# Optimization experiments

Hardware: AMD Instinct MI355X
Metric: run time of the kernel (lower is better)

## Reference

```python
import jax, jax.numpy as jnp
import numpy as np

B, C, H, W = 8, 512, 48, 48
DK = C // 8            # query/key dim
L = max(H, W)          # rel_pos_length == H == W
R = 2 * L - 1          # num relative shifts
N = H * W
EPS = 1e-5


def setup_inputs() -> dict:
    key = jax.random.key(0)
    ks = jax.random.split(key, 20)
    d = {
        "x": jax.random.normal(ks[0], (B, C, H, W), jnp.float32),
        "Wq": jax.random.normal(ks[1], (DK, C), jnp.float32) * 0.02,
        "bq": jnp.zeros((DK,), jnp.float32),
        "q_scale": jnp.ones((DK,), jnp.float32),
        "q_bias": jnp.zeros((DK,), jnp.float32),
        "Wk": jax.random.normal(ks[2], (DK, C), jnp.float32) * 0.02,
        "bk": jnp.zeros((DK,), jnp.float32),
        "k_scale": jnp.ones((DK,), jnp.float32),
        "k_bias": jnp.zeros((DK,), jnp.float32),
        "Wv": jax.random.normal(ks[3], (C, C), jnp.float32) * 0.02,
        "bv": jnp.zeros((C,), jnp.float32),
        "v_scale": jnp.ones((C,), jnp.float32),
        "v_bias": jnp.zeros((C,), jnp.float32),
        "rel_rows": jax.random.normal(ks[4], (R, DK), jnp.float32),
        "rel_columns": jax.random.normal(ks[5], (R, DK), jnp.float32),
        "bnr_scale": jnp.ones((C,), jnp.float32),
        "bnr_bias": jnp.zeros((C,), jnp.float32),
        "bnc_scale": jnp.ones((C,), jnp.float32),
        "bnc_bias": jnp.zeros((C,), jnp.float32),
        # gamma is a learned scalar (init 0 in torch; nonzero here so output != x)
        "gamma": jax.random.normal(ks[6], (1,), jnp.float32) * 0.1,
    }
    return d


def _bn(y, scale, bias):
    # train-mode BatchNorm2d: batch stats over (B,H,W), biased variance
    m = jnp.mean(y, axis=(0, 2, 3))
    v = jnp.mean((y - m[None, :, None, None]) ** 2, axis=(0, 2, 3))
    yn = (y - m[None, :, None, None]) * jax.lax.rsqrt(v + EPS)[None, :, None, None]
    return yn * scale[None, :, None, None] + bias[None, :, None, None]


def _conv_bn_relu(x, Wc, bc, scale, bias):
    y = jnp.einsum('bchw,oc->bohw', x, Wc) + bc[None, :, None, None]  # 1x1 conv
    return jax.nn.relu(_bn(y, scale, bias))


def _rel_P(l, rel_table):
    # compute_reindexing_tensor reduces to a one-hot over shift (i - x) since
    # |i-x| <= L always holds when L == l; Ih @ rel_table == gather by shift.
    x = jnp.arange(l)[:, None]
    i = jnp.arange(l)[None, :]
    idx = i - x + (L - 1)                 # (l, l) in [0, 2L-2]
    return rel_table[idx]                 # (l, l, DK)


def reference(x, Wq, bq, q_scale, q_bias, Wk, bk, k_scale, k_bias,
              Wv, bv, v_scale, v_bias, rel_rows, rel_columns,
              bnr_scale, bnr_bias, bnc_scale, bnc_bias, gamma):
    q = _conv_bn_relu(x, Wq, bq, q_scale, q_bias).reshape(B, DK, N)   # proj_query^T
    k = _conv_bn_relu(x, Wk, bk, k_scale, k_bias).reshape(B, DK, N)
    v = _conv_bn_relu(x, Wv, bv, v_scale, v_bias).reshape(B, C, N)

    energy = jnp.einsum('bdn,bdm->bnm', q, k)        # (B,N,N) = Q^T K (unscaled)
    attention = jax.nn.softmax(energy, axis=-1)
    out = jnp.einsum('bcj,bij->bci', v, attention)   # V A^T
    attn_mask = out.reshape(B, C, H, W)

    # relative position terms: Eh = V (Ph Q^T), Ew = V (Pw Q^T)
    Ph = _rel_P(H, rel_rows).reshape(N, DK)          # (N,DK) since H==W
    Mh = jnp.einsum('nd,bdm->bnm', Ph, q)
    Eh = jnp.einsum('bcn,bnm->bcm', v, Mh).reshape(B, C, H, W)
    Eh = _bn(Eh, bnr_scale, bnr_bias)

    Pw = _rel_P(W, rel_columns).reshape(N, DK)
    Mw = jnp.einsum('nd,bdm->bnm', Pw, q)
    Ew = jnp.einsum('bcn,bnm->bcm', v, Mw).reshape(B, C, H, W)
    Ew = _bn(Ew, bnc_scale, bnc_bias)

    attn_mask = attn_mask + Eh + Ew
    return gamma[0] * attn_mask + x
```

## Files before the change

kernel.cpp:

```cpp
#include <hip/hip_runtime.h>
#include <math.h>

#define BB   8
#define CIN  512
#define NSP  2304
#define OCH  640
#define LL   48

typedef __attribute__((ext_vector_type(8))) short bf16x8;
typedef __attribute__((ext_vector_type(4))) float f32x4;

__device__ inline unsigned short f2bf(float f) {
  unsigned int u = __float_as_uint(f);
  unsigned int r = (u + 0x7fffu + ((u >> 16) & 1u)) >> 16;
  return (unsigned short)r;
}
__device__ inline float bf2f(unsigned short h) {
  return __uint_as_float(((unsigned int)h) << 16);
}

#define STAGE128x64(GP, LD, LDSN)                                              \
  {                                                                            \
    const unsigned short* gsrc_ = (GP);                                        \
    _Pragma("unroll") for (int cc_ = 0; cc_ < 4; cc_++) {                      \
      int base_ = w * 2048 + cc_ * 512;                                        \
      int row_ = w * 32 + cc_ * 8 + rsub;                                      \
      __builtin_amdgcn_global_load_lds(                                        \
          (const __attribute__((address_space(1))) void*)(gsrc_ +              \
              (size_t)row_ * (LD) + colb),                                     \
          (__attribute__((address_space(3))) void*)&LDSN[base_], 16, 0, 0);    \
    }                                                                          \
  }

#define MFMA128x128x64()                                                       \
  _Pragma("unroll") for (int kk_ = 0; kk_ < 2; kk_++) {                        \
    bf16x8 af_[4], bf_[4];                                                     \
    int kcol_ = kk_ * 32 + (lane >> 4) * 8;                                    \
    _Pragma("unroll") for (int m_ = 0; m_ < 4; m_++)                           \
      af_[m_] = *(const bf16x8*)&As[(wr * 64 + m_ * 16 + (lane & 15)) * 64 + kcol_]; \
    _Pragma("unroll") for (int n_ = 0; n_ < 4; n_++)                           \
      bf_[n_] = *(const bf16x8*)&Bs[(wc * 64 + n_ * 16 + (lane & 15)) * 64 + kcol_]; \
    _Pragma("unroll") for (int m_ = 0; m_ < 4; m_++)                           \
      _Pragma("unroll") for (int n_ = 0; n_ < 4; n_++)                         \
        acc[m_][n_] = __builtin_amdgcn_mfma_f32_16x16x32_bf16(                 \
            af_[m_], bf_[n_], acc[m_][n_], 0, 0, 0);                           \
  }

#define MFMA_PROLOG()                                                          \
  const int tid = threadIdx.x;                                                 \
  const int lane = tid & 63;                                                   \
  const int w = tid >> 6;                                                      \
  const int wr = w >> 1, wc = w & 1;                                           \
  const int colb = (lane & 7) * 8;                                             \
  const int rsub = lane >> 3;                                                  \
  f32x4 acc[4][4] = {};                                                        \
  (void)colb; (void)rsub;

__global__ __launch_bounds__(256) void stack_wb(
    const float* __restrict__ Wq, const float* __restrict__ bq,
    const float* __restrict__ Wk, const float* __restrict__ bk,
    const float* __restrict__ Wv, const float* __restrict__ bv,
    unsigned short* __restrict__ Wstb, float* __restrict__ bst) {
  int idx = blockIdx.x * 256 + threadIdx.x;
  int row = idx >> 9;
  float val;
  if (row < 64)       val = Wq[idx];
  else if (row < 128) val = Wk[idx - (64 << 9)];
  else                val = Wv[idx - (128 << 9)];
  Wstb[idx] = f2bf(val);
  if (idx < OCH) {
    float bval;
    if (idx < 64)       bval = bq[idx];
    else if (idx < 128) bval = bk[idx - 64];
    else                bval = bv[idx - 128];
    bst[idx] = bval;
  }
}

__global__ __launch_bounds__(256) void prep_pcat(
    const float* __restrict__ rel_rows, const float* __restrict__ rel_cols,
    unsigned short* __restrict__ Pcatb) {
  int idx = blockIdx.x * 256 + threadIdx.x;
  int dd = idx / NSP;
  int n = idx - dd * NSP;
  int xr = n / LL;
  int ic = n - xr * LL;
  int shift = ic - xr + (LL - 1);
  float val = (dd < 64) ? rel_rows[shift * 64 + dd] : rel_cols[shift * 64 + (dd - 64)];
  Pcatb[idx] = f2bf(val);
}

__global__ __launch_bounds__(256) void transpose_x(
    const float* __restrict__ x, unsigned short* __restrict__ xTb) {
  __shared__ float t[64][65];
  const int n0 = blockIdx.x * 64;
  const int c0 = blockIdx.y * 64;
  const int b = blockIdx.z;
  const int j = threadIdx.x & 63;
  const int g = threadIdx.x >> 6;
  const float* xp = x + (size_t)b * CIN * NSP;
#pragma unroll
  for (int i = 0; i < 16; i++) {
    int cl = g * 16 + i;
    t[cl][j] = xp[(size_t)(c0 + cl) * NSP + n0 + j];
  }
  __syncthreads();
  unsigned short* op = xTb + (size_t)b * NSP * CIN;
#pragma unroll
  for (int i = 0; i < 16; i++) {
    int nl = g * 16 + i;
    op[(size_t)(n0 + nl) * CIN + c0 + j] = f2bf(t[j][nl]);
  }
}

__global__ __launch_bounds__(256) void proj_mfma(
    const unsigned short* __restrict__ Wstb, const float* __restrict__ bst,
    const unsigned short* __restrict__ xTb, unsigned short* __restrict__ y16,
    float* __restrict__ part1, float* __restrict__ part2) {
  __shared__ unsigned short As[128 * 64];
  __shared__ unsigned short Bs[128 * 64];
  int sw = ((blockIdx.x & 7) * 90) + (blockIdx.x >> 3);
  const int rb = sw % 5;
  const int nb = (sw / 5) % 18;
  const int b = sw / 90;
  const int r0 = rb * 128;
  const int n0 = nb * 128;
  MFMA_PROLOG();
  const unsigned short* A = Wstb + (size_t)r0 * CIN;
  const unsigned short* B = xTb + (size_t)b * NSP * CIN + (size_t)n0 * CIN;
  for (int k0 = 0; k0 < CIN; k0 += 64) {
    STAGE128x64(A + k0, CIN, As);
    STAGE128x64(B + k0, CIN, Bs);
    __syncthreads();
    MFMA128x128x64();
    __syncthreads();
  }
  float* sp = (float*)As;
#pragma unroll
  for (int m = 0; m < 4; m++) {
#pragma unroll
    for (int r = 0; r < 4; r++) {
      int rl = wr * 64 + m * 16 + (lane >> 4) * 4 + r;
      int row = r0 + rl;
      float bias = bst[row];
      float s1 = 0.f, s2 = 0.f;
#pragma unroll
      for (int n = 0; n < 4; n++) {
        float yv = acc[m][n][r] + bias;
        s1 += yv;
        s2 += yv * yv;
        y16[((size_t)b * OCH + row) * NSP + n0 + wc * 64 + n * 16 + (lane & 15)] = f2bf(yv);
      }
#pragma unroll
      for (int off = 1; off < 16; off <<= 1) {
        s1 += __shfl_xor(s1, off);
        s2 += __shfl_xor(s2, off);
      }
      if ((lane & 15) == 0) {
        sp[rl * 2 + wc] = s1;
        sp[256 + rl * 2 + wc] = s2;
      }
    }
  }
  __syncthreads();
  if (tid < 128) {
    size_t pbase = ((size_t)b * 18 + nb) * OCH + r0 + tid;
    part1[pbase] = sp[tid * 2] + sp[tid * 2 + 1];
    part2[pbase] = sp[256 + tid * 2] + sp[256 + tid * 2 + 1];
  }
}

__global__ __launch_bounds__(256) void bn_finalize(
    const float* __restrict__ part1, const float* __restrict__ part2,
    const float* __restrict__ qs_, const float* __restrict__ qb_,
    const float* __restrict__ ks_, const float* __restrict__ kb_,
    const float* __restrict__ vs_, const float* __restrict__ vb_,
    float* __restrict__ chanA, float* __restrict__ chanB) {
  const int ch = blockIdx.x;
  const int tid = threadIdx.x;
  float s1 = 0.f, s2 = 0.f;
  for (int t = tid; t < 144; t += 256) {
    s1 += part1[(size_t)t * OCH + ch];
    s2 += part2[(size_t)t * OCH + ch];
  }
  __shared__ float sb[8];
#pragma unroll
  for (int off = 32; off > 0; off >>= 1) {
    s1 += __shfl_down(s1, off);
    s2 += __shfl_down(s2, off);
  }
  int lane = tid & 63, wid = tid >> 6;
  if (lane == 0) { sb[wid] = s1; sb[4 + wid] = s2; }
  __syncthreads();
  if (tid == 0) {
    float ts  = sb[0] + sb[1] + sb[2] + sb[3];
    float ts2 = sb[4] + sb[5] + sb[6] + sb[7];
    const float inv = 1.f / (float)(BB * NSP);
    float mean = ts * inv;
    float var  = ts2 * inv - mean * mean;
    float scale, bias;
    if (ch < 64)       { scale = qs_[ch];       bias = qb_[ch]; }
    else if (ch < 128) { scale = ks_[ch - 64];  bias = kb_[ch - 64]; }
    else               { scale = vs_[ch - 128]; bias = vb_[ch - 128]; }
    float a = scale * rsqrtf(var + 1e-5f);
    chanA[ch] = a;
    chanB[ch] = bias - mean * a;
  }
}

__global__ __launch_bounds__(256) void bnrelu_all(
    unsigned short* __restrict__ y16, const float* __restrict__ chanA,
    const float* __restrict__ chanB) {
  size_t i = ((size_t)blockIdx.x * 256 + threadIdx.x) * 8;
  int ch = (int)((i / NSP) % OCH);
  float a = chanA[ch], bo = chanB[ch];
  ushort4 u0 = *(ushort4*)&y16[i];
  ushort4 u1 = *(ushort4*)&y16[i + 4];
  ushort4 o0, o1;
  o0.x = f2bf(fmaxf(0.f, a * bf2f(u0.x) + bo));
  o0.y = f2bf(fmaxf(0.f, a * bf2f(u0.y) + bo));
  o0.z = f2bf(fmaxf(0.f, a * bf2f(u0.z) + bo));
  o0.w = f2bf(fmaxf(0.f, a * bf2f(u0.w) + bo));
  o1.x = f2bf(fmaxf(0.f, a * bf2f(u1.x) + bo));
  o1.y = f2bf(fmaxf(0.f, a * bf2f(u1.y) + bo));
  o1.z = f2bf(fmaxf(0.f, a * bf2f(u1.z) + bo));
  o1.w = f2bf(fmaxf(0.f, a * bf2f(u1.w) + bo));
  *(ushort4*)&y16[i] = o0;
  *(ushort4*)&y16[i + 4] = o1;
}

__global__ __launch_bounds__(256) void tr_qk(
    const unsigned short* __restrict__ y16, unsigned short* __restrict__ qTb,
    unsigned short* __restrict__ kTb) {
  __shared__ unsigned short t[64][72];
  const int n0 = blockIdx.x * 64;
  const int qk = blockIdx.y;
  const int b = blockIdx.z;
  const int j = threadIdx.x & 63;
  const int g = threadIdx.x >> 6;
#pragma unroll
  for (int i = 0; i < 16; i++) {
    int cl = g * 16 + i;
    t[cl][j] = y16[((size_t)b * OCH + qk * 64 + cl) * NSP + n0 + j];
  }
  __syncthreads();
  unsigned short* out = (qk == 0) ? qTb : kTb;
#pragma unroll
  for (int i = 0; i < 16; i++) {
    int nl = g * 16 + i;
    out[((size_t)b * NSP + n0 + nl) * 64 + j] = t[j][nl];
  }
}

__global__ __launch_bounds__(256) void qsum_kernel(
    const unsigned short* __restrict__ y16, float* __restrict__ qs) {
  int bd = blockIdx.x;
  int b = bd >> 6, d = bd & 63;
  const ushort4* p = (const ushort4*)(y16 + ((size_t)b * OCH + d) * NSP);
  float s = 0.f;
  for (int t = threadIdx.x; t < NSP / 4; t += 256) {
    ushort4 u = p[t];
    s += bf2f(u.x) + bf2f(u.y) + bf2f(u.z) + bf2f(u.w);
  }
  __shared__ float sb[4];
#pragma unroll
  for (int off = 32; off > 0; off >>= 1) s += __shfl_down(s, off);
  int lane = threadIdx.x & 63, wid = threadIdx.x >> 6;
  if (lane == 0) sb[wid] = s;
  __syncthreads();
  if (threadIdx.x == 0) qs[bd] = sb[0] + sb[1] + sb[2] + sb[3];
}

__global__ __launch_bounds__(256) void gq_mfma(
    const unsigned short* __restrict__ y16, float* __restrict__ Gq) {
  __shared__ float wlds[4 * 4096];
  const int b = blockIdx.x;
  const int tid = threadIdx.x;
  const int lane = tid & 63;
  const int w = tid >> 6;
  const unsigned short* q = y16 + (size_t)b * OCH * NSP;
  f32x4 acc[4][4] = {};
  const int kbase = w * 576;
  for (int k0 = 0; k0 < 576; k0 += 32) {
    bf16x8 fr[4];
#pragma unroll
    for (int f = 0; f < 4; f++) {
      int row = f * 16 + (lane & 15);
      fr[f] = *(const bf16x8*)&q[(size_t)row * NSP + kbase + k0 + (lane >> 4) * 8];
    }
#pragma unroll
    for (int fm = 0; fm < 4; fm++)
#pragma unroll
      for (int fn = 0; fn < 4; fn++)
        acc[fm][fn] = __builtin_amdgcn_mfma_f32_16x16x32_bf16(
            fr[fm], fr[fn], acc[fm][fn], 0, 0, 0);
  }
#pragma unroll
  for (int fm = 0; fm < 4; fm++)
#pragma unroll
    for (int fn = 0; fn < 4; fn++)
#pragma unroll
      for (int r = 0; r < 4; r++) {
        int d = fm * 16 + (lane >> 4) * 4 + r;
        int e = fn * 16 + (lane & 15);
        wlds[w * 4096 + d * 64 + e] = acc[fm][fn][r];
      }
  __syncthreads();
  for (int t = tid; t < 4096; t += 256)
    Gq[(size_t)b * 4096 + t] =
        wlds[t] + wlds[4096 + t] + wlds[8192 + t] + wlds[12288 + t];
}

__global__ __launch_bounds__(256) void energy_mfma(
    const unsigned short* __restrict__ qTb, const unsigned short* __restrict__ kTb,
    unsigned short* __restrict__ Pp, float* __restrict__ Ppart) {
  __shared__ unsigned short As[128 * 64];
  __shared__ unsigned short Bs[128 * 64];
  int sw = ((blockIdx.x & 7) * 324) + (blockIdx.x >> 3);
  const int jb = sw % 18;
  const int ib = (sw / 18) % 18;
  const int b = sw / 324;
  const int i0 = ib * 128;
  const int j0 = jb * 128;
  MFMA_PROLOG();
  STAGE128x64(qTb + (size_t)b * NSP * 64 + (size_t)i0 * 64, 64, As);
  STAGE128x64(kTb + (size_t)b * NSP * 64 + (size_t)j0 * 64, 64, Bs);
  __syncthreads();
  MFMA128x128x64();
  __syncthreads();
  float* sp = (float*)As;
  unsigned short* pp = Pp + (size_t)b * NSP * NSP;
#pragma unroll
  for (int m = 0; m < 4; m++) {
#pragma unroll
    for (int r = 0; r < 4; r++) {
      int rl = wr * 64 + m * 16 + (lane >> 4) * 4 + r;
      int i = i0 + rl;
      float s1 = 0.f;
#pragma unroll
      for (int n = 0; n < 4; n++) {
        int j = j0 + wc * 64 + n * 16 + (lane & 15);
        unsigned short h = f2bf(__expf(acc[m][n][r]));
        pp[(size_t)i * NSP + j] = h;
        s1 += bf2f(h);
      }
#pragma unroll
      for (int off = 1; off < 16; off <<= 1) s1 += __shfl_xor(s1, off);
      if ((lane & 15) == 0) sp[rl * 2 + wc] = s1;
    }
  }
  __syncthreads();
  if (tid < 128)
    Ppart[((size_t)b * 18 + jb) * NSP + i0 + tid] = sp[tid * 2] + sp[tid * 2 + 1];
}

__global__ __launch_bounds__(256) void zred_kernel(
    const float* __restrict__ Ppart, float* __restrict__ rZ) {
  int row = blockIdx.x * 256 + threadIdx.x;
  int b = row / NSP, i = row % NSP;
  float s = 0.f;
#pragma unroll
  for (int jb = 0; jb < 18; jb++) s += Ppart[((size_t)b * 18 + jb) * NSP + i];
  rZ[row] = 1.f / s;
}

__global__ __launch_bounds__(256) void up_mfma(
    const unsigned short* __restrict__ y16, const unsigned short* __restrict__ Pcatb,
    float* __restrict__ Upart) {
  __shared__ unsigned short As[128 * 64];
  __shared__ unsigned short Bs[128 * 64];
  int sw = ((blockIdx.x & 7) * 24) + (blockIdx.x >> 3);
  const int cb = sw % 4;
  const int kc = (sw / 4) % 6;
  const int b = sw / 24;
  const int c0 = cb * 128;
  MFMA_PROLOG();
  const unsigned short* A = y16 + ((size_t)b * OCH + 128 + c0) * NSP;
  for (int k0 = kc * 384; k0 < kc * 384 + 384; k0 += 64) {
    STAGE128x64(A + k0, NSP, As);
    STAGE128x64(Pcatb + k0, NSP, Bs);
    __syncthreads();
    MFMA128x128x64();
    __syncthreads();
  }
  float* up = Upart + ((size_t)kc * BB + b) * CIN * 128 + (size_t)c0 * 128;
#pragma unroll
  for (int m = 0; m < 4; m++)
#pragma unroll
    for (int r = 0; r < 4; r++) {
      int rl = wr * 64 + m * 16 + (lane >> 4) * 4 + r;
#pragma unroll
      for (int n = 0; n < 4; n++) {
        int col = wc * 64 + n * 16 + (lane & 15);
        up[(size_t)rl * 128 + col] = acc[m][n][r];
      }
    }
}

__global__ __launch_bounds__(256) void up_reduce(
    const float* __restrict__ Upart, float* __restrict__ Ucat) {
  size_t idx = (size_t)blockIdx.x * 256 + threadIdx.x;
  float s = 0.f;
#pragma unroll
  for (int kc = 0; kc < 6; kc++) s += Upart[(size_t)kc * 524288 + idx];
  Ucat[idx] = s;
}

__global__ __launch_bounds__(64) void rel_stats(
    const float* __restrict__ Ucat, const float* __restrict__ Gq,
    const float* __restrict__ qs,
    const float* __restrict__ bnr_s, const float* __restrict__ bnr_b,
    const float* __restrict__ bnc_s, const float* __restrict__ bnc_b,
    float* __restrict__ gh, float* __restrict__ gw, float* __restrict__ offc) {
  const int c = blockIdx.x;
  const int d = threadIdx.x;
  __shared__ float su[2][64];
  float s1h = 0.f, s2h = 0.f, s1w = 0.f, s2w = 0.f;
  for (int b = 0; b < BB; b++) {
    size_t base = ((size_t)b * CIN + c) * 128;
    float uh = Ucat[base + d];
    float uw = Ucat[base + 64 + d];
    __syncthreads();
    su[0][d] = uh;
    su[1][d] = uw;
    __syncthreads();
    const float* G = Gq + (size_t)b * 4096 + d * 64;
    float th = 0.f, tw = 0.f;
    for (int e = 0; e < 64; e++) {
      float g = G[e];
      th += g * su[0][e];
      tw += g * su[1][e];
    }
    float qsd = qs[b * 64 + d];
    s1h += uh * qsd;
    s2h += uh * th;
    s1w += uw * qsd;
    s2w += uw * tw;
  }
#pragma unroll
  for (int off = 32; off > 0; off >>= 1) {
    s1h += __shfl_down(s1h, off);
    s2h += __shfl_down(s2h, off);
    s1w += __shfl_down(s1w, off);
    s2w += __shfl_down(s2w, off);
  }
  if (d == 0) {
    const float inv = 1.f / (float)(BB * NSP);
    float mh = s1h * inv, vh = s2h * inv - mh * mh;
    float mw = s1w * inv, vw = s2w * inv - mw * mw;
    float gch = bnr_s[c] * rsqrtf(vh + 1e-5f);
    float gcw = bnc_s[c] * rsqrtf(vw + 1e-5f);
    gh[c] = gch;
    gw[c] = gcw;
    offc[c] = (bnr_b[c] - mh * gch) + (bnc_b[c] - mw * gcw);
  }
}

__global__ __launch_bounds__(256) void combine_u(
    const float* __restrict__ Ucat, const float* __restrict__ gh,
    const float* __restrict__ gw, unsigned short* __restrict__ Ucb) {
  int idx = blockIdx.x * 256 + threadIdx.x;
  int d = idx & 63;
  int c = (idx >> 6) & 511;
  int b = idx >> 15;
  size_t base = ((size_t)b * CIN + c) * 128;
  Ucb[idx] = f2bf(Ucat[base + d] * gh[c] + Ucat[base + 64 + d] * gw[c]);
}

__global__ __launch_bounds__(256) void attn_fused_gemm(
    const unsigned short* __restrict__ y16,
    const unsigned short* __restrict__ Pp,
    const float* __restrict__ rZ,
    const unsigned short* __restrict__ Ucb,
    const unsigned short* __restrict__ qTb,
    const float* __restrict__ offc,
    const float* __restrict__ gammap,
    const float* __restrict__ x,
    float* __restrict__ dst) {
  __shared__ unsigned short As[128 * 64];
  __shared__ unsigned short Bs[128 * 64];
  int sw = ((blockIdx.x & 7) * 72) + (blockIdx.x >> 3);
  const int cb = sw % 4;
  const int ib = (sw / 4) % 18;
  const int b = sw / 72;
  const int c0 = cb * 128;
  const int i0 = ib * 128;
  MFMA_PROLOG();
  const unsigned short* A = y16 + ((size_t)b * OCH + 128 + c0) * NSP;
  const unsigned short* B = Pp + (size_t)b * NSP * NSP + (size_t)i0 * NSP;

  for (int j0 = 0; j0 < NSP; j0 += 64) {
    STAGE128x64(A + j0, NSP, As);
    STAGE128x64(B + j0, NSP, Bs);
    __syncthreads();
    MFMA128x128x64();
    __syncthreads();
  }

#pragma unroll
  for (int n = 0; n < 4; n++) {
    float rz = rZ[(size_t)b * NSP + i0 + wc * 64 + n * 16 + (lane & 15)];
#pragma unroll
    for (int m = 0; m < 4; m++)
#pragma unroll
      for (int r = 0; r < 4; r++) acc[m][n][r] *= rz;
  }

  STAGE128x64(Ucb + (size_t)b * CIN * 64 + (size_t)c0 * 64, 64, As);
  STAGE128x64(qTb + (size_t)b * NSP * 64 + (size_t)i0 * 64, 64, Bs);
  __syncthreads();
  MFMA128x128x64();

  const float gmm = gammap[0];
  const float* xp = x + (size_t)b * CIN * NSP;
  float* dp = dst + (size_t)b * CIN * NSP;
#pragma unroll
  for (int m = 0; m < 4; m++) {
#pragma unroll
    for (int r = 0; r < 4; r++) {
      int c = c0 + wr * 64 + m * 16 + (lane >> 4) * 4 + r;
      float off = offc[c];
#pragma unroll
      for (int n = 0; n < 4; n++) {
        int i = i0 + wc * 64 + n * 16 + (lane & 15);
        size_t o = (size_t)c * NSP + i;
        dp[o] = gmm * (acc[m][n][r] + off) + xp[o];
      }
    }
  }
}

extern "C" void kernel_launch(void* const* d_in, const int* in_sizes, int n_in,
                              void* d_out, int out_size, void* d_ws, size_t ws_size,
                              hipStream_t stream) {
  const float* x        = (const float*)d_in[0];
  const float* Wq       = (const float*)d_in[1];
  const float* bq       = (const float*)d_in[2];
  const float* q_scale  = (const float*)d_in[3];
  const float* q_bias   = (const float*)d_in[4];
  const float* Wk       = (const float*)d_in[5];
  const float* bk       = (const float*)d_in[6];
  const float* k_scale  = (const float*)d_in[7];
  const float* k_bias   = (const float*)d_in[8];
  const float* Wv       = (const float*)d_in[9];
  const float* bv       = (const float*)d_in[10];
  const float* v_scale  = (const float*)d_in[11];
  const float* v_bias   = (const float*)d_in[12];
  const float* rel_rows = (const float*)d_in[13];
  const float* rel_cols = (const float*)d_in[14];
  const float* bnr_s    = (const float*)d_in[15];
  const float* bnr_b    = (const float*)d_in[16];
  const float* bnc_s    = (const float*)d_in[17];
  const float* bnc_b    = (const float*)d_in[18];
  const float* gamma    = (const float*)d_in[19];
  float* dst = (float*)d_out;

  float* ws = (float*)d_ws;
  size_t o = 0;
  unsigned short* Wstb = (unsigned short*)(ws + o); o += (size_t)OCH * CIN / 2;
  float* bst    = ws + o; o += 1024;
  float* chanA  = ws + o; o += 1024;
  float* chanB  = ws + o; o += 1024;
  unsigned short* Pcatb = (unsigned short*)(ws + o); o += (size_t)128 * NSP / 2;
  unsigned short* y16 = (unsigned short*)(ws + o); o += (size_t)BB * OCH * NSP / 2;
  unsigned short* xTb = (unsigned short*)(ws + o); o += (size_t)BB * NSP * CIN / 2;
  unsigned short* Pp  = (unsigned short*)(ws + o); o += (size_t)BB * NSP * NSP / 2;
  float* Ppart  = ws + o; o += (size_t)BB * 18 * NSP;
  float* rZ     = ws + o; o += (size_t)BB * NSP;
  float* Upart  = ws + o; o += (size_t)6 * BB * CIN * 128;
  float* Ucat   = ws + o; o += (size_t)BB * CIN * 128;
  float* Gq     = ws + o; o += (size_t)BB * 64 * 64;
  float* part1  = ws + o; o += (size_t)BB * 18 * OCH;
  float* part2  = ws + o; o += (size_t)BB * 18 * OCH;
  float* qs     = ws + o; o += 1024;
  float* gh     = ws + o; o += 1024;
  float* gw     = ws + o; o += 1024;
  float* offc   = ws + o; o += 1024;
  unsigned short* qTb = (unsigned short*)(ws + o); o += (size_t)BB * NSP * 64 / 2;
  unsigned short* kTb = (unsigned short*)(ws + o); o += (size_t)BB * NSP * 64 / 2;
  unsigned short* Ucb = (unsigned short*)(ws + o); o += (size_t)BB * CIN * 64 / 2;

  stack_wb<<<(OCH * CIN) / 256, 256, 0, stream>>>(Wq, bq, Wk, bk, Wv, bv, Wstb, bst);
  prep_pcat<<<(128 * NSP) / 256, 256, 0, stream>>>(rel_rows, rel_cols, Pcatb);
  transpose_x<<<dim3(NSP / 64, CIN / 64, BB), 256, 0, stream>>>(x, xTb);

  proj_mfma<<<720, 256, 0, stream>>>(Wstb, bst, xTb, y16, part1, part2);
  bn_finalize<<<OCH, 256, 0, stream>>>(part1, part2, q_scale, q_bias, k_scale,
                                       k_bias, v_scale, v_bias, chanA, chanB);
  bnrelu_all<<<(int)((size_t)BB * OCH * NSP / 8 / 256), 256, 0, stream>>>(y16, chanA, chanB);
  tr_qk<<<dim3(NSP / 64, 2, BB), 256, 0, stream>>>(y16, qTb, kTb);
  qsum_kernel<<<BB * 64, 256, 0, stream>>>(y16, qs);
  gq_mfma<<<BB, 256, 0, stream>>>(y16, Gq);

  energy_mfma<<<2592, 256, 0, stream>>>(qTb, kTb, Pp, Ppart);
  zred_kernel<<<BB * NSP / 256, 256, 0, stream>>>(Ppart, rZ);

  up_mfma<<<192, 256, 0, stream>>>(y16, Pcatb, Upart);
  up_reduce<<<2048, 256, 0, stream>>>(Upart, Ucat);
  rel_stats<<<CIN, 64, 0, stream>>>(Ucat, Gq, qs, bnr_s, bnr_b, bnc_s, bnc_b,
                                    gh, gw, offc);
  combine_u<<<(BB * CIN * 64) / 256, 256, 0, stream>>>(Ucat, gh, gw, Ucb);

  attn_fused_gemm<<<576, 256, 0, stream>>>(y16, Pp, rZ, Ucb, qTb, offc, gamma, x, dst);
}
```

Baseline: 253.5 us.

## Double-buffer LDS in GEMM kernels, stage energy stores, split Gq, fuse prep kernels

Adds double-buffered LDS staging to proj_mfma, up_mfma and attn_fused_gemm so the next tile's global-to-LDS loads overlap the current MFMA step, and removes one barrier per iteration. The final Ucb/qTb tile is prefetched inside the main attention loop. energy_mfma now writes the exp tile to LDS first and then issues coalesced 16-byte global stores. gq_mfma is split across 4 blocks per batch with partial outputs that rel_stats sums, and the two prep kernels are merged into one launch. Doubling the LDS buffers raises shared memory per block, which may lower occupancy.

```diff
diff --git a/kernel.cpp b/kernel.cpp
--- a/kernel.cpp
+++ b/kernel.cpp
@@ -8,6 +8,7 @@
 #define LL   48
 
 typedef __attribute__((ext_vector_type(8))) short bf16x8;
+typedef __attribute__((ext_vector_type(8))) unsigned short u16x8;
 typedef __attribute__((ext_vector_type(4))) float f32x4;
 
 __device__ inline unsigned short f2bf(float f) {
@@ -28,18 +29,18 @@
       __builtin_amdgcn_global_load_lds(                                        \
           (const __attribute__((address_space(1))) void*)(gsrc_ +              \
               (size_t)row_ * (LD) + colb),                                     \
-          (__attribute__((address_space(3))) void*)&LDSN[base_], 16, 0, 0);    \
+          (__attribute__((address_space(3))) void*)&(LDSN)[base_], 16, 0, 0);  \
     }                                                                          \
   }
 
-#define MFMA128x128x64()                                                       \
+#define MFMA_STEP(APTR, BPTR)                                                  \
   _Pragma("unroll") for (int kk_ = 0; kk_ < 2; kk_++) {                        \
     bf16x8 af_[4], bf_[4];                                                     \
     int kcol_ = kk_ * 32 + (lane >> 4) * 8;                                    \
     _Pragma("unroll") for (int m_ = 0; m_ < 4; m_++)                           \
-      af_[m_] = *(const bf16x8*)&As[(wr * 64 + m_ * 16 + (lane & 15)) * 64 + kcol_]; \
+      af_[m_] = *(const bf16x8*)&(APTR)[(wr * 64 + m_ * 16 + (lane & 15)) * 64 + kcol_]; \
     _Pragma("unroll") for (int n_ = 0; n_ < 4; n_++)                           \
-      bf_[n_] = *(const bf16x8*)&Bs[(wc * 64 + n_ * 16 + (lane & 15)) * 64 + kcol_]; \
+      bf_[n_] = *(const bf16x8*)&(BPTR)[(wc * 64 + n_ * 16 + (lane & 15)) * 64 + kcol_]; \
     _Pragma("unroll") for (int m_ = 0; m_ < 4; m_++)                           \
       _Pragma("unroll") for (int n_ = 0; n_ < 4; n_++)                         \
         acc[m_][n_] = __builtin_amdgcn_mfma_f32_16x16x32_bf16(                 \
@@ -56,38 +57,39 @@
   f32x4 acc[4][4] = {};                                                        \
   (void)colb; (void)rsub;
 
-__global__ __launch_bounds__(256) void stack_wb(
+__global__ __launch_bounds__(256) void prep_all(
     const float* __restrict__ Wq, const float* __restrict__ bq,
     const float* __restrict__ Wk, const float* __restrict__ bk,
     const float* __restrict__ Wv, const float* __restrict__ bv,
-    unsigned short* __restrict__ Wstb, float* __restrict__ bst) {
-  int idx = blockIdx.x * 256 + threadIdx.x;
-  int row = idx >> 9;
-  float val;
-  if (row < 64)       val = Wq[idx];
-  else if (row < 128) val = Wk[idx - (64 << 9)];
-  else                val = Wv[idx - (128 << 9)];
-  Wstb[idx] = f2bf(val);
-  if (idx < OCH) {
-    float bval;
-    if (idx < 64)       bval = bq[idx];
-    else if (idx < 128) bval = bk[idx - 64];
-    else                bval = bv[idx - 128];
-    bst[idx] = bval;
-  }
-}
-
-__global__ __launch_bounds__(256) void prep_pcat(
     const float* __restrict__ rel_rows, const float* __restrict__ rel_cols,
+    unsigned short* __restrict__ Wstb, float* __restrict__ bst,
     unsigned short* __restrict__ Pcatb) {
   int idx = blockIdx.x * 256 + threadIdx.x;
-  int dd = idx / NSP;
-  int n = idx - dd * NSP;
-  int xr = n / LL;
-  int ic = n - xr * LL;
-  int shift = ic - xr + (LL - 1);
-  float val = (dd < 64) ? rel_rows[shift * 64 + dd] : rel_cols[shift * 64 + (dd - 64)];
-  Pcatb[idx] = f2bf(val);
+  if (idx < OCH * CIN) {
+    int row = idx >> 9;
+    float val;
+    if (row < 64)       val = Wq[idx];
+    else if (row < 128) val = Wk[idx - (64 << 9)];
+    else                val = Wv[idx - (128 << 9)];
+    Wstb[idx] = f2bf(val);
+    if (idx < OCH) {
+      float bval;
+      if (idx < 64)       bval = bq[idx];
+      else if (idx < 128) bval = bk[idx - 64];
+      else                bval = bv[idx - 128];
+      bst[idx] = bval;
+    }
+  } else {
+    int p = idx - OCH * CIN;
+    int dd = p / NSP;
+    int n = p - dd * NSP;
+    int xr = n / LL;
+    int ic = n - xr * LL;
+    int shift = ic - xr + (LL - 1);
+    float val = (dd < 64) ? rel_rows[shift * 64 + dd]
+                          : rel_cols[shift * 64 + (dd - 64)];
+    Pcatb[p] = f2bf(val);
+  }
 }
 
 __global__ __launch_bounds__(256) void transpose_x(
@@ -117,8 +119,8 @@
     const unsigned short* __restrict__ Wstb, const float* __restrict__ bst,
     const unsigned short* __restrict__ xTb, unsigned short* __restrict__ y16,
     float* __restrict__ part1, float* __restrict__ part2) {
-  __shared__ unsigned short As[128 * 64];
-  __shared__ unsigned short Bs[128 * 64];
+  __shared__ unsigned short As[2][8192];
+  __shared__ unsigned short Bs[2][8192];
   int sw = ((blockIdx.x & 7) * 90) + (blockIdx.x >> 3);
   const int rb = sw % 5;
   const int nb = (sw / 5) % 18;
@@ -128,14 +130,20 @@
   MFMA_PROLOG();
   const unsigned short* A = Wstb + (size_t)r0 * CIN;
   const unsigned short* B = xTb + (size_t)b * NSP * CIN + (size_t)n0 * CIN;
-  for (int k0 = 0; k0 < CIN; k0 += 64) {
-    STAGE128x64(A + k0, CIN, As);
-    STAGE128x64(B + k0, CIN, Bs);
+  int cur = 0;
+  STAGE128x64(A, CIN, As[0]);
+  STAGE128x64(B, CIN, Bs[0]);
+  __syncthreads();
+  for (int t = 0; t < 7; ++t) {
+    STAGE128x64(A + (t + 1) * 64, CIN, As[cur ^ 1]);
+    STAGE128x64(B + (t + 1) * 64, CIN, Bs[cur ^ 1]);
+    MFMA_STEP(As[cur], Bs[cur]);
     __syncthreads();
-    MFMA128x128x64();
-    __syncthreads();
-  }
-  float* sp = (float*)As;
+    cur ^= 1;
+  }
+  MFMA_STEP(As[cur], Bs[cur]);
+  __syncthreads();
+  float* sp = (float*)&As[0][0];
 #pragma unroll
   for (int m = 0; m < 4; m++) {
 #pragma unroll
@@ -272,21 +280,21 @@
 }
 
 __global__ __launch_bounds__(256) void gq_mfma(
-    const unsigned short* __restrict__ y16, float* __restrict__ Gq) {
+    const unsigned short* __restrict__ y16, float* __restrict__ Gqp) {
   __shared__ float wlds[4 * 4096];
-  const int b = blockIdx.x;
+  const int bx = blockIdx.x;
+  const int b = bx >> 2, kc = bx & 3;
   const int tid = threadIdx.x;
   const int lane = tid & 63;
   const int w = tid >> 6;
   const unsigned short* q = y16 + (size_t)b * OCH * NSP;
   f32x4 acc[4][4] = {};
-  const int kbase = w * 576;
-  for (int k0 = 0; k0 < 576; k0 += 32) {
+  for (int k0 = kc * 576 + w * 32; k0 < (kc + 1) * 576; k0 += 128) {
     bf16x8 fr[4];
 #pragma unroll
     for (int f = 0; f < 4; f++) {
       int row = f * 16 + (lane & 15);
-      fr[f] = *(const bf16x8*)&q[(size_t)row * NSP + kbase + k0 + (lane >> 4) * 8];
+      fr[f] = *(const bf16x8*)&q[(size_t)row * NSP + k0 + (lane >> 4) * 8];
     }
 #pragma unroll
     for (int fm = 0; fm < 4; fm++)
@@ -307,15 +315,15 @@
       }
   __syncthreads();
   for (int t = tid; t < 4096; t += 256)
-    Gq[(size_t)b * 4096 + t] =
+    Gqp[(size_t)bx * 4096 + t] =
         wlds[t] + wlds[4096 + t] + wlds[8192 + t] + wlds[12288 + t];
 }
 
 __global__ __launch_bounds__(256) void energy_mfma(
     const unsigned short* __restrict__ qTb, const unsigned short* __restrict__ kTb,
     unsigned short* __restrict__ Pp, float* __restrict__ Ppart) {
-  __shared__ unsigned short As[128 * 64];
-  __shared__ unsigned short Bs[128 * 64];
+  __shared__ unsigned short lds[16384];
+  __shared__ float rs[256];
   int sw = ((blockIdx.x & 7) * 324) + (blockIdx.x >> 3);
   const int jb = sw % 18;
   const int ib = (sw / 18) % 18;
@@ -323,35 +331,39 @@
   const int i0 = ib * 128;
   const int j0 = jb * 128;
   MFMA_PROLOG();
-  STAGE128x64(qTb + (size_t)b * NSP * 64 + (size_t)i0 * 64, 64, As);
-  STAGE128x64(kTb + (size_t)b * NSP * 64 + (size_t)j0 * 64, 64, Bs);
-  __syncthreads();
-  MFMA128x128x64();
-  __syncthreads();
-  float* sp = (float*)As;
-  unsigned short* pp = Pp + (size_t)b * NSP * NSP;
+  STAGE128x64(qTb + ((size_t)b * NSP + i0) * 64, 64, lds);
+  STAGE128x64(kTb + ((size_t)b * NSP + j0) * 64, 64, (lds + 8192));
+  __syncthreads();
+  MFMA_STEP(lds, (lds + 8192));
+  __syncthreads();
 #pragma unroll
   for (int m = 0; m < 4; m++) {
 #pragma unroll
     for (int r = 0; r < 4; r++) {
       int rl = wr * 64 + m * 16 + (lane >> 4) * 4 + r;
-      int i = i0 + rl;
       float s1 = 0.f;
 #pragma unroll
       for (int n = 0; n < 4; n++) {
-        int j = j0 + wc * 64 + n * 16 + (lane & 15);
         unsigned short h = f2bf(__expf(acc[m][n][r]));
-        pp[(size_t)i * NSP + j] = h;
+        lds[rl * 128 + wc * 64 + n * 16 + (lane & 15)] = h;
         s1 += bf2f(h);
       }
 #pragma unroll
       for (int off = 1; off < 16; off <<= 1) s1 += __shfl_xor(s1, off);
-      if ((lane & 15) == 0) sp[rl * 2 + wc] = s1;
-    }
-  }
-  __syncthreads();
+      if ((lane & 15) == 0) rs[rl * 2 + wc] = s1;
+    }
+  }
+  __syncthreads();
+  unsigned short* pp = Pp + (size_t)b * NSP * NSP;
+#pragma unroll
+  for (int c8 = tid; c8 < 2048; c8 += 256) {
+    int il = c8 >> 4;
+    int jl = (c8 & 15) * 8;
+    u16x8 v = *(const u16x8*)&lds[il * 128 + jl];
+    *(u16x8*)&pp[(size_t)(i0 + il) * NSP + j0 + jl] = v;
+  }
   if (tid < 128)
-    Ppart[((size_t)b * 18 + jb) * NSP + i0 + tid] = sp[tid * 2] + sp[tid * 2 + 1];
+    Ppart[((size_t)b * 18 + jb) * NSP + i0 + tid] = rs[tid * 2] + rs[tid * 2 + 1];
 }
 
 __global__ __launch_bounds__(256) void zred_kernel(
@@ -367,22 +379,28 @@
 __global__ __launch_bounds__(256) void up_mfma(
     const unsigned short* __restrict__ y16, const unsigned short* __restrict__ Pcatb,
     float* __restrict__ Upart) {
-  __shared__ unsigned short As[128 * 64];
-  __shared__ unsigned short Bs[128 * 64];
+  __shared__ unsigned short As[2][8192];
+  __shared__ unsigned short Bs[2][8192];
   int sw = ((blockIdx.x & 7) * 24) + (blockIdx.x >> 3);
   const int cb = sw % 4;
   const int kc = (sw / 4) % 6;
   const int b = sw / 24;
   const int c0 = cb * 128;
   MFMA_PROLOG();
-  const unsigned short* A = y16 + ((size_t)b * OCH + 128 + c0) * NSP;
-  for (int k0 = kc * 384; k0 < kc * 384 + 384; k0 += 64) {
-    STAGE128x64(A + k0, NSP, As);
-    STAGE128x64(Pcatb + k0, NSP, Bs);
+  const unsigned short* A = y16 + ((size_t)b * OCH + 128 + c0) * NSP + kc * 384;
+  const unsigned short* B = Pcatb + kc * 384;
+  int cur = 0;
+  STAGE128x64(A, NSP, As[0]);
+  STAGE128x64(B, NSP, Bs[0]);
+  __syncthreads();
+  for (int t = 0; t < 5; ++t) {
+    STAGE128x64(A + (t + 1) * 64, NSP, As[cur ^ 1]);
+    STAGE128x64(B + (t + 1) * 64, NSP, Bs[cur ^ 1]);
+    MFMA_STEP(As[cur], Bs[cur]);
     __syncthreads();
-    MFMA128x128x64();
-    __syncthreads();
-  }
+    cur ^= 1;
+  }
+  MFMA_STEP(As[cur], Bs[cur]);
   float* up = Upart + ((size_t)kc * BB + b) * CIN * 128 + (size_t)c0 * 128;
 #pragma unroll
   for (int m = 0; m < 4; m++)
@@ -407,7 +425,7 @@
 }
 
 __global__ __launch_bounds__(64) void rel_stats(
-    const float* __restrict__ Ucat, const float* __restrict__ Gq,
+    const float* __restrict__ Ucat, const float* __restrict__ Gqp,
     const float* __restrict__ qs,
     const float* __restrict__ bnr_s, const float* __restrict__ bnr_b,
     const float* __restrict__ bnc_s, const float* __restrict__ bnc_b,
@@ -424,12 +442,15 @@
     su[0][d] = uh;
     su[1][d] = uw;
     __syncthreads();
-    const float* G = Gq + (size_t)b * 4096 + d * 64;
     float th = 0.f, tw = 0.f;
-    for (int e = 0; e < 64; e++) {
-      float g = G[e];
-      th += g * su[0][e];
-      tw += g * su[1][e];
+#pragma unroll
+    for (int kc = 0; kc < 4; kc++) {
+      const float* G = Gqp + ((size_t)(b * 4 + kc)) * 4096 + d * 64;
+      for (int e = 0; e < 64; e++) {
+        float g = G[e];
+        th += g * su[0][e];
+        tw += g * su[1][e];
+      }
     }
     float qsd = qs[b * 64 + d];
     s1h += uh * qsd;
@@ -477,8 +498,8 @@
     const float* __restrict__ gammap,
     const float* __restrict__ x,
     float* __restrict__ dst) {
-  __shared__ unsigned short As[128 * 64];
-  __shared__ unsigned short Bs[128 * 64];
+  __shared__ unsigned short As[2][8192];
+  __shared__ unsigned short Bs[2][8192];
   int sw = ((blockIdx.x & 7) * 72) + (blockIdx.x >> 3);
   const int cb = sw % 4;
   const int ib = (sw / 4) % 18;
@@ -489,12 +510,21 @@
   const unsigned short* A = y16 + ((size_t)b * OCH + 128 + c0) * NSP;
   const unsigned short* B = Pp + (size_t)b * NSP * NSP + (size_t)i0 * NSP;
 
-  for (int j0 = 0; j0 < NSP; j0 += 64) {
-    STAGE128x64(A + j0, NSP, As);
-    STAGE128x64(B + j0, NSP, Bs);
+  int cur = 0;
+  STAGE128x64(A, NSP, As[0]);
+  STAGE128x64(B, NSP, Bs[0]);
+  __syncthreads();
+  for (int t = 0; t < 36; ++t) {
+    if (t < 35) {
+      STAGE128x64(A + (t + 1) * 64, NSP, As[cur ^ 1]);
+      STAGE128x64(B + (t + 1) * 64, NSP, Bs[cur ^ 1]);
+    } else {
+      STAGE128x64(Ucb + (size_t)b * CIN * 64 + (size_t)c0 * 64, 64, As[cur ^ 1]);
+      STAGE128x64(qTb + (size_t)b * NSP * 64 + (size_t)i0 * 64, 64, Bs[cur ^ 1]);
+    }
+    MFMA_STEP(As[cur], Bs[cur]);
     __syncthreads();
-    MFMA128x128x64();
-    __syncthreads();
+    cur ^= 1;
   }
 
 #pragma unroll
@@ -506,10 +536,7 @@
       for (int r = 0; r < 4; r++) acc[m][n][r] *= rz;
   }
 
-  STAGE128x64(Ucb + (size_t)b * CIN * 64 + (size_t)c0 * 64, 64, As);
-  STAGE128x64(qTb + (size_t)b * NSP * 64 + (size_t)i0 * 64, 64, Bs);
-  __syncthreads();
-  MFMA128x128x64();
+  MFMA_STEP(As[cur], Bs[cur]);
 
   const float gmm = gammap[0];
   const float* xp = x + (size_t)b * CIN * NSP;
@@ -569,7 +596,7 @@
   float* rZ     = ws + o; o += (size_t)BB * NSP;
   float* Upart  = ws + o; o += (size_t)6 * BB * CIN * 128;
   float* Ucat   = ws + o; o += (size_t)BB * CIN * 128;
-  float* Gq     = ws + o; o += (size_t)BB * 64 * 64;
+  float* Gqp    = ws + o; o += (size_t)32 * 4096;
   float* part1  = ws + o; o += (size_t)BB * 18 * OCH;
   float* part2  = ws + o; o += (size_t)BB * 18 * OCH;
   float* qs     = ws + o; o += 1024;
@@ -580,8 +607,8 @@
   unsigned short* kTb = (unsigned short*)(ws + o); o += (size_t)BB * NSP * 64 / 2;
   unsigned short* Ucb = (unsigned short*)(ws + o); o += (size_t)BB * CIN * 64 / 2;
 
-  stack_wb<<<(OCH * CIN) / 256, 256, 0, stream>>>(Wq, bq, Wk, bk, Wv, bv, Wstb, bst);
-  prep_pcat<<<(128 * NSP) / 256, 256, 0, stream>>>(rel_rows, rel_cols, Pcatb);
+  prep_all<<<(OCH * CIN + 128 * NSP) / 256, 256, 0, stream>>>(
+      Wq, bq, Wk, bk, Wv, bv, rel_rows, rel_cols, Wstb, bst, Pcatb);
   transpose_x<<<dim3(NSP / 64, CIN / 64, BB), 256, 0, stream>>>(x, xTb);
 
   proj_mfma<<<720, 256, 0, stream>>>(Wstb, bst, xTb, y16, part1, part2);
@@ -590,14 +617,14 @@
   bnrelu_all<<<(int)((size_t)BB * OCH * NSP / 8 / 256), 256, 0, stream>>>(y16, chanA, chanB);
   tr_qk<<<dim3(NSP / 64, 2, BB), 256, 0, stream>>>(y16, qTb, kTb);
   qsum_kernel<<<BB * 64, 256, 0, stream>>>(y16, qs);
-  gq_mfma<<<BB, 256, 0, stream>>>(y16, Gq);
+  gq_mfma<<<32, 256, 0, stream>>>(y16, Gqp);
 
   energy_mfma<<<2592, 256, 0, stream>>>(qTb, kTb, Pp, Ppart);
   zred_kernel<<<BB * NSP / 256, 256, 0, stream>>>(Ppart, rZ);
 
   up_mfma<<<192, 256, 0, stream>>>(y16, Pcatb, Upart);
   up_reduce<<<2048, 256, 0, stream>>>(Upart, Ucat);
-  rel_stats<<<CIN, 64, 0, stream>>>(Ucat, Gq, qs, bnr_s, bnr_b, bnc_s, bnc_b,
+  rel_stats<<<CIN, 64, 0, stream>>>(Ucat, Gqp, qs, bnr_s, bnr_b, bnc_s, bnc_b,
                                     gh, gw, offc);
   combine_u<<<(BB * CIN * 64) / 256, 256, 0, stream>>>(Ucat, gh, gw, Ucb);
 
```

Measured after the change: 293.0 us. 1.16x slower.
